# Performance work log

Measured on AMD Instinct MI355X. Metric: run time of the kernel, lower is better.

The kernel has to match this reference:

```python
import jax, jax.numpy as jnp
import numpy as np

N, D_IN, H, D_EMB = 2048, 128, 256, 64


def setup_inputs() -> dict:
    key = jax.random.key(0)
    ks = jax.random.split(key, 8)
    x = jax.random.normal(ks[0], (N, D_IN), dtype=jnp.float32)
    adj = jnp.zeros((N, N), dtype=jnp.float32)  # only its last dim is used (eye sizing)
    s = 0.05
    W0 = jax.random.normal(ks[1], (D_IN, H), dtype=jnp.float32) * s
    b0 = jnp.zeros((H,), dtype=jnp.float32)
    W1 = jax.random.normal(ks[2], (H, D_EMB), dtype=jnp.float32) * s
    b1 = jnp.zeros((D_EMB,), dtype=jnp.float32)
    W2 = jax.random.normal(ks[3], (D_IN, D_IN), dtype=jnp.float32) * s
    b2 = jnp.zeros((D_IN,), dtype=jnp.float32)
    temp = jnp.float32(0.1)
    theta = jnp.float32(0.1)
    return {"x": x, "adj": adj, "W0": W0, "b0": b0, "W1": W1, "b1": b1,
            "W2": W2, "b2": b2, "temp": temp, "theta": theta}


def reference(x, adj, W0, b0, W1, b1, W2, b2, temp, theta):
    # layer 0 (on x) and middle layer 1 (on out_x), both with ReLU activation
    out_x = jax.nn.relu(x @ W0 + b0)            # [N, H]
    emb = jax.nn.relu(out_x @ W1 + b1)          # [N, D_EMB]
    # last layer is applied to the ORIGINAL x (per the `x = model(x)` branch)
    x_last = x @ W2 + b2                        # [N, D_IN]

    # dist[i,j] = -||emb_i - emb_j||^2, computed via the gemm expansion
    sq = jnp.sum(emb * emb, axis=1)             # [N]
    dist = -(sq[:, None] + sq[None, :] - 2.0 * (emb @ emb.T))  # [N, N]

    prob = jax.nn.sigmoid((1.0 + temp) * dist + (5.0 + theta))
    A = prob + jnp.eye(adj.shape[-1], dtype=prob.dtype)        # [N, N]

    # diag(A.sum(-1))^{-1} @ A @ x_last  ==  rowwise divide by degree
    deg = jnp.sum(A, axis=-1)                   # [N]
    out = jax.nn.relu((A @ x_last) / deg[:, None])

    # sigmoid(.) > 0 everywhere, so all N*N entries are nonzero: adj_wts is the
    # full flattened adjacency (data-independent shape, jit-safe)
    adj_wts = A.reshape(-1)
    return out, adj_wts
```

## Files before the change

kernel.cpp:

```cpp
#include <hip/hip_runtime.h>
#include <hip/hip_bf16.h>


typedef short bf16x8 __attribute__((ext_vector_type(8)));
typedef float f32x4 __attribute__((ext_vector_type(4)));

__device__ __forceinline__ unsigned short f2bf(float f) {
    unsigned u = __float_as_uint(f);
    unsigned r = u + 0x7fffu + ((u >> 16) & 1u);
    return (unsigned short)(r >> 16);
}

__device__ __forceinline__ bf16x8 pack_rne8(const float* p) {
    union { unsigned u[4]; bf16x8 v; } r;
    #pragma unroll
    for (int i = 0; i < 4; ++i) {
        unsigned lo = __float_as_uint(p[2 * i]) + 0x8000u;
        unsigned hi = __float_as_uint(p[2 * i + 1]) + 0x8000u;
        r.u[i] = __builtin_amdgcn_perm(hi, lo, 0x07060302u);
    }
    return r.v;
}

__device__ __forceinline__ bf16x8 pack_bf8(const float* p) {
    union { unsigned u[4]; bf16x8 v; } r;
    #pragma unroll
    for (int i = 0; i < 4; ++i)
        r.u[i] = __builtin_amdgcn_perm(__float_as_uint(p[2 * i + 1]),
                                       __float_as_uint(p[2 * i]), 0x07060302u);
    return r.v;
}

__global__ __launch_bounds__(512, 2) void k1_mfma(
    const float* __restrict__ x,
    const float* __restrict__ W0, const float* __restrict__ b0,
    const float* __restrict__ W1, const float* __restrict__ b1,
    const float* __restrict__ W2, const float* __restrict__ b2,
    unsigned short* __restrict__ emb_bf,
    unsigned short* __restrict__ xlT_bf,
    float* __restrict__ sq)
{
    constexpr int LDO = 264;
    __shared__ unsigned short oxb[16 * LDO];
    __shared__ float sqs[4][16];

    const int t = threadIdx.x;
    const int lane = t & 63;
    const int w = t >> 6;
    const int m = lane & 15;
    const int q = lane >> 4;
    const int i0 = blockIdx.x * 16;

    bf16x8 ax[4];
    #pragma unroll
    for (int kb = 0; kb < 4; ++kb) {
        float xf[8];
        *(f32x4*)&xf[0] = *(const f32x4*)(x + (size_t)(i0 + m) * 128 + kb * 32 + q * 8);
        *(f32x4*)&xf[4] = *(const f32x4*)(x + (size_t)(i0 + m) * 128 + kb * 32 + q * 8 + 4);
        ax[kb] = pack_rne8(xf);
    }

    bf16x8 wp[8];
    float bias2 = 0.f;
    if (w < 4) {
        const int h = w * 16 + m;
        bias2 = b1[h];
        #pragma unroll
        for (int kb = 0; kb < 8; ++kb) {
            float wf[8];
            #pragma unroll
            for (int j = 0; j < 8; ++j) wf[j] = W1[(size_t)(kb * 32 + q * 8 + j) * 64 + h];
            wp[kb] = pack_rne8(wf);
        }
    } else {
        const int w2 = w - 4;
        #pragma unroll
        for (int hh = 0; hh < 2; ++hh) {
            const int c = (w2 * 2 + hh) * 16 + m;
            #pragma unroll
            for (int kb = 0; kb < 4; ++kb) {
                float wf[8];
                #pragma unroll
                for (int j = 0; j < 8; ++j) wf[j] = W2[(size_t)(kb * 32 + q * 8 + j) * 128 + c];
                wp[hh * 4 + kb] = pack_rne8(wf);
            }
        }
    }

    #pragma unroll
    for (int hh = 0; hh < 2; ++hh) {
        const int h = (w * 2 + hh) * 16 + m;
        float bb = b0[h];
        f32x4 acc = {bb, bb, bb, bb};
        #pragma unroll
        for (int kb = 0; kb < 4; ++kb) {
            float wf[8];
            #pragma unroll
            for (int j = 0; j < 8; ++j) wf[j] = W0[(size_t)(kb * 32 + q * 8 + j) * 256 + h];
            acc = __builtin_amdgcn_mfma_f32_16x16x32_bf16(ax[kb], pack_rne8(wf), acc, 0, 0, 0);
        }
        #pragma unroll
        for (int r = 0; r < 4; ++r)
            oxb[(q * 4 + r) * LDO + h] = f2bf(fmaxf(acc[r], 0.0f));
    }
    __syncthreads();

    if (w < 4) {
        const int h = w * 16 + m;
        f32x4 acc = {bias2, bias2, bias2, bias2};
        #pragma unroll
        for (int kb = 0; kb < 8; ++kb) {
            bf16x8 af = *(const bf16x8*)(&oxb[m * LDO + kb * 32 + q * 8]);
            acc = __builtin_amdgcn_mfma_f32_16x16x32_bf16(af, wp[kb], acc, 0, 0, 0);
        }
        float s2[4];
        #pragma unroll
        for (int r = 0; r < 4; ++r) {
            float e = fmaxf(acc[r], 0.0f);
            emb_bf[(size_t)(i0 + q * 4 + r) * 64 + h] = f2bf(e);
            s2[r] = e * e;
        }
        #pragma unroll
        for (int r = 0; r < 4; ++r) {
            float v = s2[r];
            v += __shfl_xor(v, 1);
            v += __shfl_xor(v, 2);
            v += __shfl_xor(v, 4);
            v += __shfl_xor(v, 8);
            if (m == 0) sqs[w][q * 4 + r] = v;
        }
    } else {
        const int w2 = w - 4;
        #pragma unroll
        for (int hh = 0; hh < 2; ++hh) {
            const int c = (w2 * 2 + hh) * 16 + m;
            float bb = b2[c];
            f32x4 acc = {bb, bb, bb, bb};
            #pragma unroll
            for (int kb = 0; kb < 4; ++kb)
                acc = __builtin_amdgcn_mfma_f32_16x16x32_bf16(ax[kb], wp[hh * 4 + kb], acc, 0, 0, 0);
            uint2 pk;
            pk.x = (unsigned)f2bf(acc[0]) | ((unsigned)f2bf(acc[1]) << 16);
            pk.y = (unsigned)f2bf(acc[2]) | ((unsigned)f2bf(acc[3]) << 16);
            *(uint2*)(&xlT_bf[(size_t)c * 2048 + i0 + q * 4]) = pk;
        }
    }
    __syncthreads();
    if (t < 16)
        sq[i0 + t] = sqs[0][t] + sqs[1][t] + sqs[2][t] + sqs[3][t];
}

__global__ __launch_bounds__(256, 2) void k2f(
    const unsigned short* __restrict__ emb_bf,
    const unsigned short* __restrict__ xlT_bf,
    const float* __restrict__ sq,
    const float* __restrict__ tempp, const float* __restrict__ thetap,
    float* __restrict__ adjw,
    float* __restrict__ outPart,
    float* __restrict__ degPart)
{
    constexpr int LDP = 132;
    __shared__ float Pt[2][16 * LDP];
    __shared__ float degS[4][16];

    const int t = threadIdx.x;
    const int lane = t & 63;
    const int w = t >> 6;
    const int m = lane & 15;
    const int q = lane >> 4;
    const int i0 = blockIdx.x * 16;
    const int bj = blockIdx.y;
    const int jstrip0 = bj * 256;
    const float scale = 1.0f + tempp[0];
    const float bias = 5.0f + thetap[0];

    bf16x8 a0 = *(const bf16x8*)(emb_bf + (size_t)(i0 + m) * 64 + q * 8);
    bf16x8 a1 = *(const bf16x8*)(emb_bf + (size_t)(i0 + m) * 64 + 32 + q * 8);
    float sqIr[4];
    #pragma unroll
    for (int r = 0; r < 4; ++r) sqIr[r] = sq[i0 + q * 4 + r];

    f32x4 accO0 = {0.f, 0.f, 0.f, 0.f};
    f32x4 accO1 = {0.f, 0.f, 0.f, 0.f};
    float dega[4] = {0.f, 0.f, 0.f, 0.f};
    const int cg = w * 32;

    #pragma unroll
    for (int jt = 0; jt < 2; ++jt) {
        const int j0 = jstrip0 + jt * 128;
        float* P = &Pt[jt][0];

        bf16x8 xb[8];
        #pragma unroll
        for (int s = 0; s < 4; ++s) {
            const int k = j0 + s * 32 + q * 8;
            xb[2 * s]     = *(const bf16x8*)(xlT_bf + (size_t)(cg + m) * 2048 + k);
            xb[2 * s + 1] = *(const bf16x8*)(xlT_bf + (size_t)(cg + 16 + m) * 2048 + k);
        }

        #pragma unroll
        for (int s = 0; s < 2; ++s) {
            const int col = (w * 2 + s) * 16 + m;
            const unsigned short* ebj = emb_bf + (size_t)(j0 + col) * 64;
            bf16x8 b0 = *(const bf16x8*)(ebj + q * 8);
            bf16x8 b1 = *(const bf16x8*)(ebj + 32 + q * 8);
            f32x4 S = {0.f, 0.f, 0.f, 0.f};
            S = __builtin_amdgcn_mfma_f32_16x16x32_bf16(a0, b0, S, 0, 0, 0);
            S = __builtin_amdgcn_mfma_f32_16x16x32_bf16(a1, b1, S, 0, 0, 0);

            const float csqJ = sq[j0 + col];
            const int gcol = j0 + col;
            #pragma unroll
            for (int r = 0; r < 4; ++r) {
                int grow = i0 + q * 4 + r;
                float dist = 2.0f * S[r] - sqIr[r] - csqJ;
                float z = scale * dist + bias;
                float p = __builtin_amdgcn_rcpf(1.0f + __expf(-z));
                if (grow == gcol) p += 1.0f;
                dega[r] += p;
                P[(q * 4 + r) * LDP + col] = p;
            }
        }
        __syncthreads();

        {
            int row = t >> 4;
            int c0 = (t & 15) * 8;
            f32x4 v0 = *(const f32x4*)(&P[row * LDP + c0]);
            f32x4 v1 = *(const f32x4*)(&P[row * LDP + c0 + 4]);
            f32x4* dst = (f32x4*)(adjw + (size_t)(i0 + row) * 2048 + j0 + c0);
            dst[0] = v0;
            dst[1] = v1;
        }

        #pragma unroll
        for (int s = 0; s < 4; ++s) {
            float af[8];
            *(f32x4*)(&af[0]) = *(const f32x4*)(&P[m * LDP + s * 32 + q * 8]);
            *(f32x4*)(&af[4]) = *(const f32x4*)(&P[m * LDP + s * 32 + q * 8 + 4]);
            bf16x8 aa = pack_bf8(af);
            accO0 = __builtin_amdgcn_mfma_f32_16x16x32_bf16(aa, xb[2 * s], accO0, 0, 0, 0);
            accO1 = __builtin_amdgcn_mfma_f32_16x16x32_bf16(aa, xb[2 * s + 1], accO1, 0, 0, 0);
        }
    }

    #pragma unroll
    for (int r = 0; r < 4; ++r) {
        float v = dega[r];
        v += __shfl_xor(v, 1);
        v += __shfl_xor(v, 2);
        v += __shfl_xor(v, 4);
        v += __shfl_xor(v, 8);
        if (m == 0) degS[w][q * 4 + r] = v;
    }
    __syncthreads();
    if (t < 16)
        degPart[bj * 2048 + i0 + t] =
            degS[0][t] + degS[1][t] + degS[2][t] + degS[3][t];

    float* op = outPart + ((size_t)bj * 2048 + i0) * 128;
    #pragma unroll
    for (int r = 0; r < 4; ++r) {
        op[(q * 4 + r) * 128 + cg + m] = accO0[r];
        op[(q * 4 + r) * 128 + cg + 16 + m] = accO1[r];
    }
}

__global__ __launch_bounds__(256) void k3_fin(
    const float* __restrict__ outPart, const float* __restrict__ degPart,
    float* __restrict__ out)
{
    int idx4 = (blockIdx.x * 256 + threadIdx.x) * 4;
    int row = idx4 >> 7;
    float4 s = make_float4(0.f, 0.f, 0.f, 0.f);
    float d = 0.f;
    #pragma unroll
    for (int p = 0; p < 8; ++p) {
        float4 v = *(const float4*)(&outPart[(size_t)p * 262144 + idx4]);
        s.x += v.x; s.y += v.y; s.z += v.z; s.w += v.w;
        d += degPart[p * 2048 + row];
    }
    float dinv = 1.0f / d;
    s.x = fmaxf(s.x * dinv, 0.f);
    s.y = fmaxf(s.y * dinv, 0.f);
    s.z = fmaxf(s.z * dinv, 0.f);
    s.w = fmaxf(s.w * dinv, 0.f);
    *(float4*)(&out[idx4]) = s;
}

extern "C" void kernel_launch(void* const* d_in, const int* in_sizes, int n_in,
                              void* d_out, int out_size, void* d_ws, size_t ws_size,
                              hipStream_t stream) {
    const float* x     = (const float*)d_in[0];
    const float* W0    = (const float*)d_in[2];
    const float* b0    = (const float*)d_in[3];
    const float* W1    = (const float*)d_in[4];
    const float* b1    = (const float*)d_in[5];
    const float* W2    = (const float*)d_in[6];
    const float* b2    = (const float*)d_in[7];
    const float* temp  = (const float*)d_in[8];
    const float* theta = (const float*)d_in[9];

    char* ws = (char*)d_ws;
    unsigned short* emb_bf = (unsigned short*)(ws);
    unsigned short* xlT_bf = (unsigned short*)(ws + 262144);
    float* sq      = (float*)(ws + 786432);
    float* degPart = (float*)(ws + 794624);
    float* outPart = (float*)(ws + 860160);

    float* out  = (float*)d_out;
    float* adjw = (float*)d_out + 262144;

    k1_mfma<<<128, 512, 0, stream>>>(x, W0, b0, W1, b1, W2, b2,
                                     emb_bf, xlT_bf, sq);
    k2f<<<dim3(128, 8), 256, 0, stream>>>(emb_bf, xlT_bf, sq, temp, theta,
                                          adjw, outPart, degPart);
    k3_fin<<<256, 256, 0, stream>>>(outPart, degPart, out);
}
```

Baseline: 110.5 us.

## Coalesce adjacency stores and repack partial outputs as contiguous float2

The adjacency tile store is remapped so each thread writes one float4 in each of two rows, and 32 threads cover a full 128-float row segment for wider contiguous writes. Partial output accumulators are stored as packed float2 in a tile-local layout so each wave writes contiguous memory rather than strided scalars. The finalize kernel is rewritten to read that new layout with two scalar accumulators per thread and launches twice as many blocks. This trades vector float4 loads and stores in the finalize step for scalar ones.

New measurement: 109.2 us. About the same (-1.2%).

```diff
diff --git a/kernel.cpp b/kernel.cpp
--- a/kernel.cpp
+++ b/kernel.cpp
@@ -224,13 +224,12 @@
         __syncthreads();
 
         {
-            int row = t >> 4;
-            int c0 = (t & 15) * 8;
+            int row = t >> 5;
+            int c0 = (t & 31) * 4;
             f32x4 v0 = *(const f32x4*)(&P[row * LDP + c0]);
-            f32x4 v1 = *(const f32x4*)(&P[row * LDP + c0 + 4]);
-            f32x4* dst = (f32x4*)(adjw + (size_t)(i0 + row) * 2048 + j0 + c0);
-            dst[0] = v0;
-            dst[1] = v1;
+            f32x4 v1 = *(const f32x4*)(&P[(row + 8) * LDP + c0]);
+            *(f32x4*)(adjw + (size_t)(i0 + row) * 2048 + j0 + c0) = v0;
+            *(f32x4*)(adjw + (size_t)(i0 + row + 8) * 2048 + j0 + c0) = v1;
         }
 
         #pragma unroll
@@ -258,11 +257,13 @@
         degPart[bj * 2048 + i0 + t] =
             degS[0][t] + degS[1][t] + degS[2][t] + degS[3][t];
 
-    float* op = outPart + ((size_t)bj * 2048 + i0) * 128;
+    float2* opf2 = (float2*)outPart + ((size_t)bj * 128 + blockIdx.x) * 1024;
     #pragma unroll
     for (int r = 0; r < 4; ++r) {
-        op[(q * 4 + r) * 128 + cg + m] = accO0[r];
-        op[(q * 4 + r) * 128 + cg + 16 + m] = accO1[r];
+        float2 pk;
+        pk.x = accO0[r];
+        pk.y = accO1[r];
+        opf2[((q * 4 + r) * 4 + w) * 16 + m] = pk;
     }
 }
 
@@ -270,22 +271,23 @@
     const float* __restrict__ outPart, const float* __restrict__ degPart,
     float* __restrict__ out)
 {
-    int idx4 = (blockIdx.x * 256 + threadIdx.x) * 4;
-    int row = idx4 >> 7;
-    float4 s = make_float4(0.f, 0.f, 0.f, 0.f);
-    float d = 0.f;
+    int gid = blockIdx.x * 256 + threadIdx.x;
+    int i = gid >> 6;
+    int wm = gid & 63;
+    int w = wm >> 4, m = wm & 15;
+    int tile = i >> 4, rit = i & 15;
+    size_t base = (size_t)tile * 2048 + (size_t)((rit * 4 + w) * 16 + m) * 2;
+    float s0 = 0.f, s1 = 0.f, d = 0.f;
     #pragma unroll
     for (int p = 0; p < 8; ++p) {
-        float4 v = *(const float4*)(&outPart[(size_t)p * 262144 + idx4]);
-        s.x += v.x; s.y += v.y; s.z += v.z; s.w += v.w;
-        d += degPart[p * 2048 + row];
+        const float* src = outPart + (size_t)p * 262144 + base;
+        s0 += src[0];
+        s1 += src[1];
+        d += degPart[p * 2048 + i];
     }
     float dinv = 1.0f / d;
-    s.x = fmaxf(s.x * dinv, 0.f);
-    s.y = fmaxf(s.y * dinv, 0.f);
-    s.z = fmaxf(s.z * dinv, 0.f);
-    s.w = fmaxf(s.w * dinv, 0.f);
-    *(float4*)(&out[idx4]) = s;
+    out[(size_t)i * 128 + w * 32 + m] = fmaxf(s0 * dinv, 0.f);
+    out[(size_t)i * 128 + w * 32 + 16 + m] = fmaxf(s1 * dinv, 0.f);
 }
 
 extern "C" void kernel_launch(void* const* d_in, const int* in_sizes, int n_in,
@@ -315,5 +317,5 @@
                                      emb_bf, xlT_bf, sq);
     k2f<<<dim3(128, 8), 256, 0, stream>>>(emb_bf, xlT_bf, sq, temp, theta,
                                           adjw, outPart, degPart);
-    k3_fin<<<256, 256, 0, stream>>>(outPart, degPart, out);
-}
+    k3_fin<<<512, 256, 0, stream>>>(outPart, degPart, out);
+}
```
